# Kernel optimization log

Hardware: AMD Instinct MI355X
Metric: run time of the kernel (lower is better)

The kernel has to match this reference:

```python
import jax, jax.numpy as jnp
import numpy as np
from jax import lax

VOCAB = 5000
BLANK = 0          # vocab.unk_id
SMOOTHING = 0.1    # config.model.label_smoothing
ALPHA = 0.2        # config.model.alpha
NEG = -1e30        # finite stand-in for -inf (stable under logaddexp)


def setup_inputs() -> dict:
    key = jax.random.key(0)
    k1, k2, k3 = jax.random.split(key, 3)
    att_logits = jax.random.normal(k1, (16, 128, VOCAB), dtype=jnp.float32)
    ctc_logits = jax.random.normal(k2, (16, 512, VOCAB), dtype=jnp.float32)
    targets = jax.random.randint(k3, (16, 128), 0, VOCAB)
    return {"att_logits": att_logits, "ctc_logits": ctc_logits, "targets": targets}


def _label_smoothing_loss(logit_bsv, targets_bs):
    # torch: label_smoothed filled with smoothing/(V-1), confidence at target;
    # loss = mean over rows of sum(-label_smoothed * logit).
    B, S, V = logit_bsv.shape
    logit = logit_bsv.reshape(-1, V)                       # (B*S, V)
    tgt = targets_bs.reshape(-1)                           # (B*S,)
    confidence = 1.0 - SMOOTHING
    off = SMOOTHING / (V - 1)
    tgt_logit = jnp.take_along_axis(logit, tgt[:, None], axis=1)[:, 0]
    row_sum = jnp.sum(logit, axis=-1)
    # sum(-ls*logit) = -(confidence*logit[t] + off*(row_sum - logit[t]))
    per_row = -(confidence * tgt_logit + off * (row_sum - tgt_logit))
    return jnp.mean(per_row)


def _ctc_loss(log_probs_btv, targets_bs):
    # torch nn.CTCLoss(blank=BLANK, reduction='mean', zero_infinity=True)
    # input is time-major log-probs (T, B, V); full lengths on both sides.
    lp = jnp.transpose(log_probs_btv, (1, 0, 2))           # (T, B, V)
    T, B, V = lp.shape
    S = targets_bs.shape[1]
    L = 2 * S + 1
    # extended target: blank interleaved
    ext = jnp.full((B, L), BLANK, dtype=targets_bs.dtype).at[:, 1::2].set(targets_bs)
    # emission log-probs per extended symbol: (T, B, L)
    emit = jnp.take_along_axis(lp, jnp.broadcast_to(ext[None], (T, B, L)), axis=2)
    # skip (s-2) transition allowed when ext[s] != blank and ext[s] != ext[s-2]
    ext_m2 = jnp.roll(ext, 2, axis=1)
    allow2 = (ext != BLANK) & (ext != ext_m2)
    allow2 = allow2.at[:, :2].set(False)
    alpha0 = jnp.full((B, L), NEG, dtype=lp.dtype)
    alpha0 = alpha0.at[:, 0].set(emit[0, :, 0]).at[:, 1].set(emit[0, :, 1])

    negpad1 = jnp.full((B, 1), NEG, dtype=lp.dtype)
    negpad2 = jnp.full((B, 2), NEG, dtype=lp.dtype)

    def step(alpha, e_t):
        a1 = jnp.concatenate([negpad1, alpha[:, :-1]], axis=1)
        a2 = jnp.concatenate([negpad2, alpha[:, :-2]], axis=1)
        a2 = jnp.where(allow2, a2, NEG)
        new = jnp.logaddexp(jnp.logaddexp(alpha, a1), a2) + e_t
        return new, None

    alphaT, _ = lax.scan(step, alpha0, emit[1:])
    ll = jnp.logaddexp(alphaT[:, L - 1], alphaT[:, L - 2])
    loss_b = -ll                                           # (B,)
    # zero_infinity: invalid paths (loss ~ 1e30) -> 0
    loss_b = jnp.where(loss_b > 1e20, 0.0, loss_b)
    # reduction='mean': divide by target length, then mean over batch
    return jnp.mean(loss_b / S)


def reference(att_logits, ctc_logits, targets):
    att_loss = _label_smoothing_loss(att_logits, targets)
    ctc_loss = _ctc_loss(ctc_logits, targets)
    return ALPHA * att_loss + (1.0 - ALPHA) * ctc_loss
```

## Files before the change

### kernel.cpp

```cpp
#include <hip/hip_runtime.h>
#include <math.h>

#define VOCAB   5000
#define T_CTC   512
#define S_TGT   128
#define BATCH   16
#define ALPHA_W 0.2f
#define CONF    0.9f
#define OFFV    (0.1f / 4999.0f)
#define CHUNK   32
#define NCHUNK  16
#define CSTR    132
#define WS_OFF  16

__global__ __launch_bounds__(256)
void gather_kernel(const float* __restrict__ ctc,
                   const int*   __restrict__ tgt,
                   float*       __restrict__ ws)
{
    const int b     = blockIdx.x >> 8;
    const int tpair = blockIdx.x & 255;
    const int t0    = 2 * tpair;

    __shared__ int tg[S_TGT];
    if (threadIdx.x < S_TGT) tg[threadIdx.x] = tgt[b * S_TGT + threadIdx.x];
    __syncthreads();

    const float* lp   = ctc + (size_t)b * T_CTC * VOCAB;
    float*       cbuf = ws + WS_OFF + ((size_t)b * T_CTC) * CSTR;

    for (int v = threadIdx.x; v < 258; v += 256) {
        const int tt  = (v < 129) ? 0 : 1;
        const int idx = (v < 129) ? v : v - 129;
        const int col = (idx < 128) ? tg[idx] : 0;
        cbuf[(size_t)(t0 + tt) * CSTR + idx] = lp[(size_t)(t0 + tt) * VOCAB + col];
    }
}

__global__ __launch_bounds__(512)
void fused_loss_kernel(const float* __restrict__ att,
                       const int*   __restrict__ tgt,
                       float*       __restrict__ ws)
{
    __shared__ __align__(16) float ebuf[2][CHUNK][CSTR];

    if (blockIdx.x < BATCH) {
        const int b    = blockIdx.x;
        const int tid  = threadIdx.x;
        const int wave = tid >> 6;
        const int lane = tid & 63;
        const int*   tg   = tgt + b * S_TGT;
        const float* cbuf = ws + WS_OFF + ((size_t)b * T_CTC) * CSTR;

        {
            const float4* src = (const float4*)(cbuf + (size_t)1 * CSTR);
            float4*       dst = (float4*)&ebuf[0][0][0];
            for (int i = tid; i < CHUNK * (CSTR / 4); i += 512) dst[i] = src[i];
        }

        const int k  = lane;
        const int t1 = tg[2 * k];
        const int t3 = tg[2 * k + 1];
        const int tp = (k > 0) ? tg[2 * k - 1] : 0;
        const double g1 = ((k > 0) && (t1 != 0) && (t1 != tp)) ? 1.0 : 0.0;
        const double g3 = ((t3 != 0) && (t3 != t1)) ? 1.0 : 0.0;

        const float e00 = cbuf[128];
        double M  = (double)e00;
        double b0 = (k == 0) ? 1.0 : 0.0;
        double b1 = (k == 0) ? (double)__expf(cbuf[0] - e00) : 0.0;
        double b2 = 0.0, b3 = 0.0, b4 = 0.0;

        __syncthreads();

        for (int c = 0; c < NCHUNK; ++c) {
            const int buf = c & 1;
            if (wave == 0) {
                const int tbase = 1 + c * CHUNK;
                #pragma unroll
                for (int i = 0; i < CHUNK; ++i) {
                    if (tbase + i < T_CTC) {
                        const float2 e13 = *reinterpret_cast<const float2*>(&ebuf[buf][i][2 * k]);
                        const float  e0  = ebuf[buf][i][128];
                        const double E1 = (double)__expf(e13.x - e0);
                        const double E3 = (double)__expf(e13.y - e0);
                        double p3 = __shfl_up(b3, 1, 64);
                        p3 = (k == 0) ? 0.0 : p3;
                        const double n0 = b0 + p3;
                        const double n1 = (b1 + b0 + g1 * p3) * E1;
                        const double n2 = b2 + b1;
                        const double n3 = (b3 + b2 + g3 * b1) * E3;
                        const double n4 = b4 + b3;
                        b0 = n0; b1 = n1; b2 = n2; b3 = n3; b4 = n4;
                        M += (double)e0;
                    }
                }
            } else if (c + 1 < NCHUNK) {
                const int nbuf  = buf ^ 1;
                const int tbase = 1 + (c + 1) * CHUNK;
                const int rows  = min(CHUNK, T_CTC - tbase);
                const float4* src = (const float4*)(cbuf + (size_t)tbase * CSTR);
                float4*       dst = (float4*)&ebuf[nbuf][0][0];
                const int n4v = rows * (CSTR / 4);
                for (int i = tid - 64; i < n4v; i += 448) dst[i] = src[i];
            }
            __syncthreads();
        }

        if (wave == 0 && k == 63) {
            const double bsum = b3 + b4;
            const double ll   = M + log(bsum);
            float loss_b = (float)(-ll);
            if (!(loss_b <= 1e20f)) loss_b = 0.0f;
            atomicAdd(&ws[1], loss_b);
        }
        return;
    }

    const int rr = blockIdx.x - BATCH;
    const float* row = att + (size_t)rr * VOCAB;
    const float4* row4 = (const float4*)row;

    float sum = 0.0f;
    for (int i = threadIdx.x; i < VOCAB / 4; i += 512) {
        float4 v = row4[i];
        sum += v.x + v.y + v.z + v.w;
    }
    #pragma unroll
    for (int off = 32; off > 0; off >>= 1)
        sum += __shfl_down(sum, off, 64);

    __shared__ float wsum[8];
    const int wv = threadIdx.x >> 6;
    if ((threadIdx.x & 63) == 0) wsum[wv] = sum;
    __syncthreads();
    if (threadIdx.x == 0) {
        float rs = 0.0f;
        #pragma unroll
        for (int i = 0; i < 8; ++i) rs += wsum[i];
        const float tl = row[tgt[rr]];
        atomicAdd(&ws[0], -(CONF * tl + OFFV * (rs - tl)));
    }
}

__global__ void combine_kernel(const float* __restrict__ ws, float* __restrict__ out)
{
    if (threadIdx.x == 0 && blockIdx.x == 0) {
        const float inv = 1.0f / (float)(BATCH * S_TGT);
        out[0] = ALPHA_W * (ws[0] * inv) + (1.0f - ALPHA_W) * (ws[1] * inv);
    }
}

extern "C" void kernel_launch(void* const* d_in, const int* in_sizes, int n_in,
                              void* d_out, int out_size, void* d_ws, size_t ws_size,
                              hipStream_t stream)
{
    const float* att = (const float*)d_in[0];
    const float* ctc = (const float*)d_in[1];
    const int*   tgt = (const int*)d_in[2];
    float* out = (float*)d_out;
    float* ws  = (float*)d_ws;

    hipMemsetAsync(ws, 0, 2 * sizeof(float), stream);
    gather_kernel<<<BATCH * (T_CTC / 2), 256, 0, stream>>>(ctc, tgt, ws);
    fused_loss_kernel<<<BATCH + BATCH * S_TGT, 512, 0, stream>>>(att, tgt, ws);
    combine_kernel<<<1, 64, 0, stream>>>(ws, out);
}
```

Baseline: 295.5 us.

## Move att row-sum into gather kernel and batch exp ahead of CTC recurrence

The attention label-smoothing row reductions now run in the gather kernel instead of alongside the 16 CTC blocks. Per-row partial losses are written to the workspace rather than accumulated atomically, so the memset goes away and a parallel combine kernel sums them. The CTC kernel now gets its own launch with chunk size 64, and it computes exps for 16 timesteps before running the serial recurrence, which takes the exp latency off the dependency chain. The trade-offs are a larger shared buffer and extra registers for the batched exps.

```diff
diff --git a/kernel.cpp b/kernel.cpp
--- a/kernel.cpp
+++ b/kernel.cpp
@@ -8,121 +8,46 @@
 #define ALPHA_W 0.2f
 #define CONF    0.9f
 #define OFFV    (0.1f / 4999.0f)
-#define CHUNK   32
-#define NCHUNK  16
+#define CHUNK   64
+#define NCHUNK  8
 #define CSTR    132
-#define WS_OFF  16
+#define ATT_N   (BATCH * S_TGT)
+#define WS_OFF  4096
+#define GATHER_BLKS (BATCH * (T_CTC / 2))
 
 __global__ __launch_bounds__(256)
-void gather_kernel(const float* __restrict__ ctc,
-                   const int*   __restrict__ tgt,
-                   float*       __restrict__ ws)
-{
-    const int b     = blockIdx.x >> 8;
-    const int tpair = blockIdx.x & 255;
-    const int t0    = 2 * tpair;
-
-    __shared__ int tg[S_TGT];
-    if (threadIdx.x < S_TGT) tg[threadIdx.x] = tgt[b * S_TGT + threadIdx.x];
-    __syncthreads();
-
-    const float* lp   = ctc + (size_t)b * T_CTC * VOCAB;
-    float*       cbuf = ws + WS_OFF + ((size_t)b * T_CTC) * CSTR;
-
-    for (int v = threadIdx.x; v < 258; v += 256) {
-        const int tt  = (v < 129) ? 0 : 1;
-        const int idx = (v < 129) ? v : v - 129;
-        const int col = (idx < 128) ? tg[idx] : 0;
-        cbuf[(size_t)(t0 + tt) * CSTR + idx] = lp[(size_t)(t0 + tt) * VOCAB + col];
-    }
-}
-
-__global__ __launch_bounds__(512)
-void fused_loss_kernel(const float* __restrict__ att,
+void gather_att_kernel(const float* __restrict__ ctc,
+                       const float* __restrict__ att,
                        const int*   __restrict__ tgt,
                        float*       __restrict__ ws)
 {
-    __shared__ __align__(16) float ebuf[2][CHUNK][CSTR];
+    if (blockIdx.x < GATHER_BLKS) {
+        const int b     = blockIdx.x >> 8;
+        const int tpair = blockIdx.x & 255;
+        const int t0    = 2 * tpair;
 
-    if (blockIdx.x < BATCH) {
-        const int b    = blockIdx.x;
-        const int tid  = threadIdx.x;
-        const int wave = tid >> 6;
-        const int lane = tid & 63;
-        const int*   tg   = tgt + b * S_TGT;
-        const float* cbuf = ws + WS_OFF + ((size_t)b * T_CTC) * CSTR;
-
-        {
-            const float4* src = (const float4*)(cbuf + (size_t)1 * CSTR);
-            float4*       dst = (float4*)&ebuf[0][0][0];
-            for (int i = tid; i < CHUNK * (CSTR / 4); i += 512) dst[i] = src[i];
-        }
-
-        const int k  = lane;
-        const int t1 = tg[2 * k];
-        const int t3 = tg[2 * k + 1];
-        const int tp = (k > 0) ? tg[2 * k - 1] : 0;
-        const double g1 = ((k > 0) && (t1 != 0) && (t1 != tp)) ? 1.0 : 0.0;
-        const double g3 = ((t3 != 0) && (t3 != t1)) ? 1.0 : 0.0;
-
-        const float e00 = cbuf[128];
-        double M  = (double)e00;
-        double b0 = (k == 0) ? 1.0 : 0.0;
-        double b1 = (k == 0) ? (double)__expf(cbuf[0] - e00) : 0.0;
-        double b2 = 0.0, b3 = 0.0, b4 = 0.0;
-
+        __shared__ int tg[S_TGT];
+        if (threadIdx.x < S_TGT) tg[threadIdx.x] = tgt[b * S_TGT + threadIdx.x];
         __syncthreads();
 
-        for (int c = 0; c < NCHUNK; ++c) {
-            const int buf = c & 1;
-            if (wave == 0) {
-                const int tbase = 1 + c * CHUNK;
-                #pragma unroll
-                for (int i = 0; i < CHUNK; ++i) {
-                    if (tbase + i < T_CTC) {
-                        const float2 e13 = *reinterpret_cast<const float2*>(&ebuf[buf][i][2 * k]);
-                        const float  e0  = ebuf[buf][i][128];
-                        const double E1 = (double)__expf(e13.x - e0);
-                        const double E3 = (double)__expf(e13.y - e0);
-                        double p3 = __shfl_up(b3, 1, 64);
-                        p3 = (k == 0) ? 0.0 : p3;
-                        const double n0 = b0 + p3;
-                        const double n1 = (b1 + b0 + g1 * p3) * E1;
-                        const double n2 = b2 + b1;
-                        const double n3 = (b3 + b2 + g3 * b1) * E3;
-                        const double n4 = b4 + b3;
-                        b0 = n0; b1 = n1; b2 = n2; b3 = n3; b4 = n4;
-                        M += (double)e0;
-                    }
-                }
-            } else if (c + 1 < NCHUNK) {
-                const int nbuf  = buf ^ 1;
-                const int tbase = 1 + (c + 1) * CHUNK;
-                const int rows  = min(CHUNK, T_CTC - tbase);
-                const float4* src = (const float4*)(cbuf + (size_t)tbase * CSTR);
-                float4*       dst = (float4*)&ebuf[nbuf][0][0];
-                const int n4v = rows * (CSTR / 4);
-                for (int i = tid - 64; i < n4v; i += 448) dst[i] = src[i];
-            }
-            __syncthreads();
-        }
+        const float* lp   = ctc + (size_t)b * T_CTC * VOCAB;
+        float*       cbuf = ws + WS_OFF + ((size_t)b * T_CTC) * CSTR;
 
-        if (wave == 0 && k == 63) {
-            const double bsum = b3 + b4;
-            const double ll   = M + log(bsum);
-            float loss_b = (float)(-ll);
-            if (!(loss_b <= 1e20f)) loss_b = 0.0f;
-            atomicAdd(&ws[1], loss_b);
+        for (int v = threadIdx.x; v < 258; v += 256) {
+            const int tt  = (v < 129) ? 0 : 1;
+            const int idx = (v < 129) ? v : v - 129;
+            const int col = (idx < 128) ? tg[idx] : 0;
+            cbuf[(size_t)(t0 + tt) * CSTR + idx] = lp[(size_t)(t0 + tt) * VOCAB + col];
         }
         return;
     }
 
-    const int rr = blockIdx.x - BATCH;
+    const int rr = blockIdx.x - GATHER_BLKS;
     const float* row = att + (size_t)rr * VOCAB;
     const float4* row4 = (const float4*)row;
 
     float sum = 0.0f;
-    for (int i = threadIdx.x; i < VOCAB / 4; i += 512) {
+    for (int i = threadIdx.x; i < VOCAB / 4; i += 256) {
         float4 v = row4[i];
         sum += v.x + v.y + v.z + v.w;
     }
@@ -130,24 +55,123 @@
     for (int off = 32; off > 0; off >>= 1)
         sum += __shfl_down(sum, off, 64);
 
-    __shared__ float wsum[8];
-    const int wv = threadIdx.x >> 6;
-    if ((threadIdx.x & 63) == 0) wsum[wv] = sum;
+    __shared__ float wsum[4];
+    if ((threadIdx.x & 63) == 0) wsum[threadIdx.x >> 6] = sum;
     __syncthreads();
     if (threadIdx.x == 0) {
-        float rs = 0.0f;
-        #pragma unroll
-        for (int i = 0; i < 8; ++i) rs += wsum[i];
+        const float rs = wsum[0] + wsum[1] + wsum[2] + wsum[3];
         const float tl = row[tgt[rr]];
-        atomicAdd(&ws[0], -(CONF * tl + OFFV * (rs - tl)));
+        ws[rr] = -(CONF * tl + OFFV * (rs - tl));
     }
 }
 
-__global__ void combine_kernel(const float* __restrict__ ws, float* __restrict__ out)
+__global__ __launch_bounds__(512)
+void ctc_kernel(const int* __restrict__ tgt, float* __restrict__ ws)
 {
-    if (threadIdx.x == 0 && blockIdx.x == 0) {
-        const float inv = 1.0f / (float)(BATCH * S_TGT);
-        out[0] = ALPHA_W * (ws[0] * inv) + (1.0f - ALPHA_W) * (ws[1] * inv);
+    __shared__ __align__(16) float ebuf[2][CHUNK][CSTR];
+
+    const int b    = blockIdx.x;
+    const int tid  = threadIdx.x;
+    const int wave = tid >> 6;
+    const int lane = tid & 63;
+    const int*   tg   = tgt + b * S_TGT;
+    const float* cbuf = ws + WS_OFF + ((size_t)b * T_CTC) * CSTR;
+
+    {
+        const float4* src = (const float4*)(cbuf + (size_t)1 * CSTR);
+        float4*       dst = (float4*)&ebuf[0][0][0];
+        for (int i = tid; i < CHUNK * (CSTR / 4); i += 512) dst[i] = src[i];
+    }
+
+    const int k  = lane;
+    const int t1 = tg[2 * k];
+    const int t3 = tg[2 * k + 1];
+    const int tp = (k > 0) ? tg[2 * k - 1] : 0;
+    const double g1 = ((k > 0) && (t1 != 0) && (t1 != tp)) ? 1.0 : 0.0;
+    const double g3 = ((t3 != 0) && (t3 != t1)) ? 1.0 : 0.0;
+
+    const float e00 = cbuf[128];
+    double M  = (double)e00;
+    double b0 = (k == 0) ? 1.0 : 0.0;
+    double b1 = (k == 0) ? (double)__expf(cbuf[0] - e00) : 0.0;
+    double b2 = 0.0, b3 = 0.0, b4 = 0.0;
+
+    __syncthreads();
+
+    for (int c = 0; c < NCHUNK; ++c) {
+        const int buf = c & 1;
+        if (wave == 0) {
+            const int tbase = 1 + c * CHUNK;
+            #pragma unroll
+            for (int h = 0; h < CHUNK / 16; ++h) {
+                double X1[16], X3[16];
+                float  Z[16];
+                #pragma unroll
+                for (int i = 0; i < 16; ++i) {
+                    const int st = h * 16 + i;
+                    const float2 e13 = *reinterpret_cast<const float2*>(&ebuf[buf][st][2 * k]);
+                    const float  e0  = ebuf[buf][st][128];
+                    X1[i] = (double)__expf(e13.x - e0);
+                    X3[i] = (double)__expf(e13.y - e0);
+                    Z[i]  = e0;
+                }
+                #pragma unroll
+                for (int i = 0; i < 16; ++i) {
+                    if (tbase + h * 16 + i < T_CTC) {
+                        double p3 = __shfl_up(b3, 1, 64);
+                        p3 = (k == 0) ? 0.0 : p3;
+                        const double n0 = b0 + p3;
+                        const double n1 = (b1 + b0 + g1 * p3) * X1[i];
+                        const double n2 = b2 + b1;
+                        const double n3 = (b3 + b2 + g3 * b1) * X3[i];
+                        const double n4 = b4 + b3;
+                        b0 = n0; b1 = n1; b2 = n2; b3 = n3; b4 = n4;
+                        M += (double)Z[i];
+                    }
+                }
+            }
+        } else if (c + 1 < NCHUNK) {
+            const int nbuf  = buf ^ 1;
+            const int tbase = 1 + (c + 1) * CHUNK;
+            const int rows  = min(CHUNK, T_CTC - tbase);
+            const float4* src = (const float4*)(cbuf + (size_t)tbase * CSTR);
+            float4*       dst = (float4*)&ebuf[nbuf][0][0];
+            const int n4v = rows * (CSTR / 4);
+            for (int i = tid - 64; i < n4v; i += 448) dst[i] = src[i];
+        }
+        __syncthreads();
+    }
+
+    if (wave == 0 && k == 63) {
+        const double bsum = b3 + b4;
+        const double ll   = M + log(bsum);
+        float loss_b = (float)(-ll);
+        if (!(loss_b <= 1e20f)) loss_b = 0.0f;
+        ws[ATT_N + b] = loss_b;
+    }
+}
+
+__global__ __launch_bounds__(256)
+void combine_kernel(const float* __restrict__ ws, float* __restrict__ out)
+{
+    const int tid = threadIdx.x;
+    float s_att = 0.0f;
+    for (int i = tid; i < ATT_N; i += 256) s_att += ws[i];
+    float s_ctc = (tid < BATCH) ? ws[ATT_N + tid] : 0.0f;
+
+    #pragma unroll
+    for (int off = 32; off > 0; off >>= 1) {
+        s_att += __shfl_down(s_att, off, 64);
+        s_ctc += __shfl_down(s_ctc, off, 64);
+    }
+    __shared__ float wa[4], wc[4];
+    if ((tid & 63) == 0) { wa[tid >> 6] = s_att; wc[tid >> 6] = s_ctc; }
+    __syncthreads();
+    if (tid == 0) {
+        const float inv = 1.0f / (float)ATT_N;
+        const float a = (wa[0] + wa[1] + wa[2] + wa[3]) * inv;
+        const float c = (wc[0] + wc[1] + wc[2] + wc[3]) * inv;
+        out[0] = ALPHA_W * a + (1.0f - ALPHA_W) * c;
     }
 }
 
@@ -161,8 +185,7 @@
     float* out = (float*)d_out;
     float* ws  = (float*)d_ws;
 
-    hipMemsetAsync(ws, 0, 2 * sizeof(float), stream);
-    gather_kernel<<<BATCH * (T_CTC / 2), 256, 0, stream>>>(ctc, tgt, ws);
-    fused_loss_kernel<<<BATCH + BATCH * S_TGT, 512, 0, stream>>>(att, tgt, ws);
-    combine_kernel<<<1, 64, 0, stream>>>(ws, out);
+    gather_att_kernel<<<GATHER_BLKS + ATT_N, 256, 0, stream>>>(ctc, att, tgt, ws);
+    ctc_kernel<<<BATCH, 512, 0, stream>>>(tgt, ws);
+    combine_kernel<<<1, 256, 0, stream>>>(ws, out);
 }
```

New measurement: 285.6 us. 1.03x faster.
